# Kernel optimization log

Hardware: AMD Instinct MI355X
Metric: run time of the kernel (lower is better)

The kernel has to match this reference:

```python
import jax, jax.numpy as jnp
import numpy as np

N_HEAD = 16
THETA = 10000.0


def _freqs_cos_sin(head_dim, seq_len):
    # matches precompute_freqs_cis: freqs = 1/theta^(arange(0,dim,2)/dim), outer with t
    inv = 1.0 / (THETA ** (jnp.arange(0, head_dim, 2, dtype=jnp.float32) / head_dim))
    t = jnp.arange(seq_len, dtype=jnp.float32)
    ang = jnp.outer(t, inv)  # [L, head_dim//2]
    return jnp.cos(ang), jnp.sin(ang)


def _rope(x, cos, sin):
    # x: [B, H, L, D]; pairs are interleaved (view_as_complex on (..., D//2, 2))
    x1 = x[..., 0::2]
    x2 = x[..., 1::2]
    out_re = x1 * cos - x2 * sin
    out_im = x1 * sin + x2 * cos
    return jnp.stack([out_re, out_im], axis=-1).reshape(x.shape)


def setup_inputs() -> dict:
    key = jax.random.key(0)
    ks = jax.random.split(key, 11)
    B, L, D = 2, 2048, 1024
    s = 0.02
    return {
        "q": jax.random.normal(ks[0], (B, L, D), jnp.float32),
        "k": jax.random.normal(ks[1], (B, L, D), jnp.float32),
        "v": jax.random.normal(ks[2], (B, L, D), jnp.float32),
        "wq": jax.random.normal(ks[3], (D, D), jnp.float32) * s,
        "bq": jax.random.normal(ks[4], (D,), jnp.float32) * s,
        "wk": jax.random.normal(ks[5], (D, D), jnp.float32) * s,
        "bk": jax.random.normal(ks[6], (D,), jnp.float32) * s,
        "wv": jax.random.normal(ks[7], (D, D), jnp.float32) * s,
        "bv": jax.random.normal(ks[8], (D,), jnp.float32) * s,
        "wo": jax.random.normal(ks[9], (D, D), jnp.float32) * s,
        "bo": jax.random.normal(ks[10], (D,), jnp.float32) * s,
    }


def reference(q, k, v, wq, bq, wk, bk, wv, bv, wo, bo):
    B, L, D = q.shape
    Hd = D // N_HEAD
    # projections (nn.Linear: x @ W^T + b)
    qp = q @ wq.T + bq
    kp = k @ wk.T + bk
    vp = v @ wv.T + bv
    # split: [B, L, D] -> [B, H, L, Hd]
    def split(t):
        return t.reshape(B, L, N_HEAD, Hd).transpose(0, 2, 1, 3)
    qh, kh, vh = split(qp), split(kp), split(vp)
    cos, sin = _freqs_cos_sin(Hd, L)  # [L, Hd//2], broadcasts over B, H
    qh = _rope(qh, cos, sin)
    kh = _rope(kh, cos, sin)
    # scaled dot-product attention (no mask)
    scores = jnp.einsum("bhqd,bhkd->bhqk", qh, kh) / jnp.sqrt(jnp.float32(Hd))
    attn = jax.nn.softmax(scores, axis=-1)
    out = jnp.einsum("bhqk,bhkd->bhqd", attn, vh)
    # concat heads and output projection
    out = out.transpose(0, 2, 1, 3).reshape(B, L, D)
    return out @ wo.T + bo
```

## Files before the change

kernel.cpp:

```cpp
#include <hip/hip_runtime.h>
#include <hip/hip_bf16.h>
#include <math.h>

#define BB 2
#define LL 2048
#define DD 1024
#define NH 16
#define HD 64

typedef short v8s __attribute__((ext_vector_type(8)));
typedef float v4f __attribute__((ext_vector_type(4)));
typedef float v16f __attribute__((ext_vector_type(16)));

__device__ __forceinline__ float b2f(unsigned short b) {
  union { unsigned int u; float f; } c; c.u = ((unsigned int)b) << 16; return c.f;
}
__device__ __forceinline__ unsigned short f2b(float x) {
  union { float f; unsigned int u; } c; c.f = x;
  unsigned int u = c.u;
  u += 0x7fffu + ((u >> 16) & 1u);
  return (unsigned short)(u >> 16);
}
__device__ __forceinline__ unsigned int asu(float x) {
  union { float f; unsigned int u; } c; c.f = x; return c.u;
}
__device__ __forceinline__ unsigned int pk2(float lo, float hi) {
  return __builtin_amdgcn_perm(asu(hi), asu(lo), 0x07060302u);
}

#if defined(__has_builtin)
#if __has_builtin(__builtin_amdgcn_exp2f)
#define EXP2(x) __builtin_amdgcn_exp2f(x)
#else
#define EXP2(x) __expf((x) * 0.69314718056f)
#endif
#else
#define EXP2(x) __expf((x) * 0.69314718056f)
#endif

__device__ __forceinline__ void gload16(const void* g, void* l) {
  __builtin_amdgcn_global_load_lds(
      (const __attribute__((address_space(1))) void*)g,
      (__attribute__((address_space(3))) void*)l, 16, 0, 0);
}

struct CastArgs { const float* s[7]; unsigned short* d[7]; float* ct; float* st; };
__global__ void cast_all(CastArgs a) {
  int z = blockIdx.z;
  if (z == 16) {
    if (blockIdx.x >= 256) return;
    int id = blockIdx.x * blockDim.x + threadIdx.x;
    int t = id >> 5, i = id & 31;
    float inv = powf(10000.0f, -(float)(2 * i) / 64.0f);
    float ang = (float)t * inv;
    a.ct[id] = cosf(ang);
    a.st[id] = sinf(ang);
    return;
  }
  int t = (z < 12) ? (z >> 2) : (z - 9);
  int off = (z < 12) ? ((z & 3) << 18) : 0;
  int i = off + blockIdx.x * blockDim.x + threadIdx.x;
  float4 v = ((const float4*)a.s[t])[i];
  ushort4 o;
  o.x = f2b(v.x); o.y = f2b(v.y); o.z = f2b(v.z); o.w = f2b(v.w);
  ((ushort4*)a.d[t])[i] = o;
}

template <typename OutT>
__device__ __forceinline__ void gemm_body(const unsigned short* __restrict__ X,
                                          const unsigned short* __restrict__ W,
                                          const float* __restrict__ bias,
                                          OutT* __restrict__ Y,
                                          int M, int N, int K) {
  __shared__ __align__(16) unsigned short LDS_[2][16384];
  const int tid = threadIdx.x;
  const int lane = tid & 63, wave = tid >> 6;
  const int quad = lane >> 4, l16 = lane & 15;
  const int bm0 = blockIdx.x * 128;
  const int bn0 = blockIdx.y * 128;
  const int wm = (wave >> 1) * 64, wn = (wave & 1) * 64;

  const v4f vzero = {0.f, 0.f, 0.f, 0.f};
  v4f acc[4][4];
#pragma unroll
  for (int i = 0; i < 4; ++i)
#pragma unroll
    for (int j = 0; j < 4; ++j) acc[i][j] = vzero;

  auto stage = [&](int buf, int k0) {
    unsigned short* As = LDS_[buf];
    unsigned short* Bs = LDS_[buf] + 8192;
#pragma unroll
    for (int c = 0; c < 4; ++c) {
      int id = c * 256 + tid;
      int r = id >> 3, cc = ((id & 7) ^ (r & 7)) * 8;
      gload16(X + (size_t)(bm0 + r) * K + k0 + cc, &As[id * 8]);
    }
#pragma unroll
    for (int c = 0; c < 4; ++c) {
      int id = c * 256 + tid;
      int r = id >> 3, cc = ((id & 7) ^ (r & 7)) * 8;
      gload16(W + (size_t)(bn0 + r) * K + k0 + cc, &Bs[id * 8]);
    }
  };

  stage(0, 0);
  const int nt = K >> 6;
  for (int t = 0; t < nt; ++t) {
    __syncthreads();
    if (t + 1 < nt) stage((t + 1) & 1, (t + 1) << 6);
    const unsigned short* As = LDS_[t & 1];
    const unsigned short* Bs = LDS_[t & 1] + 8192;
#pragma unroll
    for (int kh = 0; kh < 2; ++kh) {
      v8s a[4], b[4];
#pragma unroll
      for (int i = 0; i < 4; ++i) {
        int ra = wm + i * 16 + l16;
        int sa = (kh * 4 + quad) ^ (ra & 7);
        a[i] = *(const v8s*)&As[ra * 64 + sa * 8];
        int rb = wn + i * 16 + l16;
        int sb = (kh * 4 + quad) ^ (rb & 7);
        b[i] = *(const v8s*)&Bs[rb * 64 + sb * 8];
      }
#pragma unroll
      for (int mi = 0; mi < 4; ++mi)
#pragma unroll
        for (int ni = 0; ni < 4; ++ni)
          acc[mi][ni] = __builtin_amdgcn_mfma_f32_16x16x32_bf16(a[mi], b[ni], acc[mi][ni], 0, 0, 0);
    }
  }

  float bv[4];
#pragma unroll
  for (int ni = 0; ni < 4; ++ni) bv[ni] = bias[bn0 + wn + ni * 16 + l16];
#pragma unroll
  for (int mi = 0; mi < 4; ++mi) {
#pragma unroll
    for (int r = 0; r < 4; ++r) {
      int row = bm0 + wm + mi * 16 + quad * 4 + r;
      size_t base = (size_t)row * N + bn0 + wn + l16;
#pragma unroll
      for (int ni = 0; ni < 4; ++ni) {
        float v = acc[mi][ni][r] + bv[ni];
        if constexpr (sizeof(OutT) == 2) {
          Y[base + ni * 16] = (OutT)f2b(v);
        } else {
          Y[base + ni * 16] = (OutT)v;
        }
      }
    }
  }
}

__global__ __launch_bounds__(256) void gemm_qkv(
    const unsigned short* __restrict__ qb, const unsigned short* __restrict__ kb,
    const unsigned short* __restrict__ vb,
    const unsigned short* __restrict__ wqb, const unsigned short* __restrict__ wkb,
    const unsigned short* __restrict__ wvb,
    const float* __restrict__ bq, const float* __restrict__ bk,
    const float* __restrict__ bv_,
    unsigned short* __restrict__ qp, unsigned short* __restrict__ khh,
    unsigned short* __restrict__ vt,
    const float* __restrict__ ctab, const float* __restrict__ stab) {
  __shared__ __align__(16) unsigned short LDS_[2][16384];
  const int z = blockIdx.z;
  const unsigned short* X = (z == 0) ? qb : (z == 1) ? kb : vb;
  const unsigned short* W = (z == 0) ? wqb : (z == 1) ? wkb : wvb;
  const float* bias = (z == 0) ? bq : (z == 1) ? bk : bv_;
  const int K = DD, N = DD;
  const int tid = threadIdx.x;
  const int lane = tid & 63, wave = tid >> 6;
  const int quad = lane >> 4, l16 = lane & 15;
  const int bm0 = blockIdx.x * 128;
  const int bn0 = blockIdx.y * 128;
  const int wm = (wave >> 1) * 64, wn = (wave & 1) * 64;

  const v4f vzero = {0.f, 0.f, 0.f, 0.f};
  v4f acc[4][4];
#pragma unroll
  for (int i = 0; i < 4; ++i)
#pragma unroll
    for (int j = 0; j < 4; ++j) acc[i][j] = vzero;

  auto stage = [&](int buf, int k0) {
    unsigned short* As = LDS_[buf];
    unsigned short* Bs = LDS_[buf] + 8192;
#pragma unroll
    for (int c = 0; c < 4; ++c) {
      int id = c * 256 + tid;
      int r = id >> 3, cc = ((id & 7) ^ (r & 7)) * 8;
      gload16(X + (size_t)(bm0 + r) * K + k0 + cc, &As[id * 8]);
    }
#pragma unroll
    for (int c = 0; c < 4; ++c) {
      int id = c * 256 + tid;
      int r = id >> 3, cc = ((id & 7) ^ (r & 7)) * 8;
      gload16(W + (size_t)(bn0 + r) * K + k0 + cc, &Bs[id * 8]);
    }
  };

  stage(0, 0);
  const int nt = K >> 6;
  for (int t = 0; t < nt; ++t) {
    __syncthreads();
    if (t + 1 < nt) stage((t + 1) & 1, (t + 1) << 6);
    const unsigned short* As = LDS_[t & 1];
    const unsigned short* Bs = LDS_[t & 1] + 8192;
#pragma unroll
    for (int kh = 0; kh < 2; ++kh) {
      v8s a[4], b[4];
#pragma unroll
      for (int i = 0; i < 4; ++i) {
        int ra = wm + i * 16 + l16;
        int sa = (kh * 4 + quad) ^ (ra & 7);
        a[i] = *(const v8s*)&As[ra * 64 + sa * 8];
        int rb = wn + i * 16 + l16;
        int sb = (kh * 4 + quad) ^ (rb & 7);
        b[i] = *(const v8s*)&Bs[rb * 64 + sb * 8];
      }
#pragma unroll
      for (int mi = 0; mi < 4; ++mi)
#pragma unroll
        for (int ni = 0; ni < 4; ++ni)
          acc[mi][ni] = __builtin_amdgcn_mfma_f32_16x16x32_bf16(a[mi], b[ni], acc[mi][ni], 0, 0, 0);
    }
  }

  float bv[4];
#pragma unroll
  for (int ni = 0; ni < 4; ++ni) bv[ni] = bias[bn0 + wn + ni * 16 + l16];

  if (z < 2) {
    const float scl = (z == 0) ? 0.18033688f : 1.0f;
    const int h = (bn0 + wn) >> 6;
    const float sgn = (l16 & 1) ? 1.0f : -1.0f;
#pragma unroll
    for (int mi = 0; mi < 4; ++mi) {
#pragma unroll
      for (int r = 0; r < 4; ++r) {
        int row = bm0 + wm + mi * 16 + quad * 4 + r;
        int l = row & (LL - 1);
        int bidx = row >> 11;
        size_t baseq = (size_t)row * N + bn0 + wn + l16;
        size_t basek = ((size_t)(bidx * NH + h) * LL + l) * HD + l16;
#pragma unroll
        for (int ni = 0; ni < 4; ++ni) {
          int ii = (ni * 16 + l16) >> 1;
          float c = ctab[l * 32 + ii], s = stab[l * 32 + ii];
          float v = acc[mi][ni][r] + bv[ni];
          float vp = __shfl_xor(v, 1);
          float o = (v * c + sgn * (vp * s)) * scl;
          if (z == 0) qp[baseq + ni * 16] = f2b(o);
          else        khh[basek + ni * 16] = f2b(o);
        }
      }
    }
  } else {
    unsigned short* T = LDS_[0];
#pragma unroll
    for (int mi = 0; mi < 4; ++mi)
#pragma unroll
      for (int r = 0; r < 4; ++r) {
        int tl = wm + mi * 16 + quad * 4 + r;
        int tlp = (tl & ~12) | ((tl & 4) << 1) | ((tl & 8) >> 1);
        int chunk = tlp >> 3, offw = tlp & 7;
#pragma unroll
        for (int ni = 0; ni < 4; ++ni) {
          int fl = wn + ni * 16 + l16;
          T[fl * 128 + ((chunk ^ (fl & 15)) * 8) + offw] =
              f2b(acc[mi][ni][r] + bv[ni]);
        }
      }
    __syncthreads();
    int fl = tid >> 1, half = tid & 1;
    int fg = bn0 + fl;
    int h2 = fg >> 6, d = fg & 63;
    int bidx = bm0 >> 11, l0 = bm0 & (LL - 1);
    unsigned short* dst =
        vt + (((size_t)(bidx * NH + h2) * HD + d) * LL) + l0 + half * 64;
#pragma unroll
    for (int i = 0; i < 8; ++i) {
      int chunk = half * 8 + i;
      int slot = chunk ^ (fl & 15);
      *(v8s*)(dst + i * 8) = *(const v8s*)&T[fl * 128 + slot * 8];
    }
  }
}

__global__ __launch_bounds__(256) void gemm_out(
    const unsigned short* x, const unsigned short* w, const float* b, float* y) {
  gemm_body<float>(x, w, b, y, BB * LL, DD, DD);
}

__global__ __launch_bounds__(256, 2) void flash_kernel(
    const unsigned short* __restrict__ qp,
    const unsigned short* __restrict__ kh,
    const unsigned short* __restrict__ vt,
    unsigned short* __restrict__ attn) {
  __shared__ __align__(16) unsigned short S_[2][16384];
  const int tid = threadIdx.x, wave = tid >> 6, lane = tid & 63;
  const int l32 = lane & 31, hf = lane >> 5;
  const int bh = blockIdx.x, b = bh >> 4, hd = bh & 15;
  const int q0 = blockIdx.y * 128;
  const unsigned short* kbase = kh + (size_t)bh * LL * HD;
  const unsigned short* vbase = vt + (size_t)bh * HD * LL;

  const int qrow = q0 + wave * 32 + l32;
  v8s qf[4];
  {
    const unsigned short* qsrc = qp + ((size_t)(b * LL + qrow) * DD + hd * HD);
#pragma unroll
    for (int ks2 = 0; ks2 < 4; ++ks2)
      qf[ks2] = *(const v8s*)(qsrc + ks2 * 16 + hf * 8);
  }

  v16f o0, o1;
#pragma unroll
  for (int i = 0; i < 16; ++i) { o0[i] = 0.0f; o1[i] = 0.0f; }
  float ls = 0.0f;

  {
    unsigned short* Kb = S_[0];
    unsigned short* Vb = S_[0] + 8192;
#pragma unroll
    for (int i = 0; i < 4; ++i) {
      int id = i * 256 + tid;
      int r = id >> 3, c = (id & 7) ^ (r & 7);
      gload16(kbase + (size_t)r * HD + c * 8, &Kb[id * 8]);
    }
#pragma unroll
    for (int i = 0; i < 4; ++i) {
      int id = i * 256 + tid;
      int r = id >> 4, c = (id & 15) ^ (r & 15);
      gload16(vbase + (size_t)r * LL + c * 8, &Vb[id * 8]);
    }
  }

  for (int t = 0; t < 16; ++t) {
    __syncthreads();
    if (t < 15) {
      int kt = (t + 1) * 128;
      unsigned short* Kb = S_[(t + 1) & 1];
      unsigned short* Vb = Kb + 8192;
#pragma unroll
      for (int i = 0; i < 4; ++i) {
        int id = i * 256 + tid;
        int r = id >> 3, c = (id & 7) ^ (r & 7);
        gload16(kbase + (size_t)(kt + r) * HD + c * 8, &Kb[id * 8]);
      }
#pragma unroll
      for (int i = 0; i < 4; ++i) {
        int id = i * 256 + tid;
        int r = id >> 4, c = (id & 15) ^ (r & 15);
        gload16(vbase + (size_t)r * LL + kt + c * 8, &Vb[id * 8]);
      }
    }
    const unsigned short* Ks = S_[t & 1];
    const unsigned short* Vs = Ks + 8192;

#pragma unroll
    for (int g = 0; g < 4; ++g) {
      v16f sc;
#pragma unroll
      for (int i = 0; i < 16; ++i) sc[i] = 0.0f;
#pragma unroll
      for (int ks2 = 0; ks2 < 4; ++ks2) {
        int row = g * 32 + l32;
        int slot = (ks2 * 2 + hf) ^ (lane & 7);
        v8s kf = *(const v8s*)&Ks[row * 64 + slot * 8];
        sc = __builtin_amdgcn_mfma_f32_32x32x16_bf16(kf, qf[ks2], sc, 0, 0, 0);
      }
      v16f e;
#pragma unroll
      for (int i = 0; i < 16; ++i) e[i] = EXP2(sc[i]);
      float t0 = (e[0] + e[1]) + (e[2] + e[3]);
      float t1 = (e[4] + e[5]) + (e[6] + e[7]);
      float t2 = (e[8] + e[9]) + (e[10] + e[11]);
      float t3 = (e[12] + e[13]) + (e[14] + e[15]);
      ls += (t0 + t1) + (t2 + t3);
#pragma unroll
      for (int k2 = 0; k2 < 2; ++k2) {
        union { v8s v; unsigned int u[4]; } pb;
#pragma unroll
        for (int a = 0; a < 4; ++a)
          pb.u[a] = pk2(e[8 * k2 + 2 * a], e[8 * k2 + 2 * a + 1]);
        int k16 = g * 2 + k2;
        int slotv = (k16 * 2 + hf) ^ (lane & 15);
        v8s vf0 = *(const v8s*)&Vs[l32 * 128 + slotv * 8];
        v8s vf1 = *(const v8s*)&Vs[(32 + l32) * 128 + slotv * 8];
        o0 = __builtin_amdgcn_mfma_f32_32x32x16_bf16(vf0, pb.v, o0, 0, 0, 0);
        o1 = __builtin_amdgcn_mfma_f32_32x32x16_bf16(vf1, pb.v, o1, 0, 0, 0);
      }
    }
  }

  ls += __shfl_xor(ls, 32);
  float inv = 1.0f / ls;

  unsigned short* Wt = S_[0] + wave * 2048;
#pragma unroll
  for (int dt = 0; dt < 2; ++dt)
#pragma unroll
    for (int r = 0; r < 16; ++r) {
      int dl = (r & 3) + 8 * (r >> 2) + 4 * hf;
      int d = dt * 32 + dl;
      int chunk = d >> 3, offw = d & 7;
      int slot = chunk ^ (l32 & 7);
      float val = (dt == 0) ? o0[r] : o1[r];
      Wt[l32 * 64 + slot * 8 + offw] = f2b(val * inv);
    }
#pragma unroll
  for (int i = 0; i < 4; ++i) {
    int qr = lane >> 1;
    int chunk = (lane & 1) * 4 + i;
    int slot = chunk ^ (qr & 7);
    v8s dv = *(const v8s*)&Wt[qr * 64 + slot * 8];
    int token = q0 + wave * 32 + qr;
    *(v8s*)(attn + ((size_t)(b * LL + token) * DD) + hd * HD + chunk * 8) = dv;
  }
}

extern "C" void kernel_launch(void* const* d_in, const int* in_sizes, int n_in,
                              void* d_out, int out_size, void* d_ws, size_t ws_size,
                              hipStream_t stream) {
  const float* q  = (const float*)d_in[0];
  const float* k  = (const float*)d_in[1];
  const float* v  = (const float*)d_in[2];
  const float* wq = (const float*)d_in[3];
  const float* bq = (const float*)d_in[4];
  const float* wk = (const float*)d_in[5];
  const float* bk = (const float*)d_in[6];
  const float* wv = (const float*)d_in[7];
  const float* bv = (const float*)d_in[8];
  const float* wo = (const float*)d_in[9];
  const float* bo = (const float*)d_in[10];
  float* out = (float*)d_out;

  size_t off = 0;
  char* wsb = (char*)d_ws;
  auto take = [&](size_t n) { void* p = wsb + off; off += n; return p; };
  const size_t SZT = (size_t)BB * LL * DD * 2;
  const size_t SZW = (size_t)DD * DD * 2;
  unsigned short* qb   = (unsigned short*)take(SZT);
  unsigned short* kb   = (unsigned short*)take(SZT);
  unsigned short* vb   = (unsigned short*)take(SZT);
  unsigned short* wqb  = (unsigned short*)take(SZW);
  unsigned short* wkb  = (unsigned short*)take(SZW);
  unsigned short* wvb  = (unsigned short*)take(SZW);
  unsigned short* wob  = (unsigned short*)take(SZW);
  unsigned short* qp   = (unsigned short*)take(SZT);
  unsigned short* khh  = (unsigned short*)take(SZT);
  unsigned short* vtt  = (unsigned short*)take(SZT);
  unsigned short* attn = (unsigned short*)take(SZT);
  float* ctab = (float*)take((size_t)LL * 32 * 4);
  float* stab = (float*)take((size_t)LL * 32 * 4);

  CastArgs ca;
  ca.s[0] = q;  ca.s[1] = k;  ca.s[2] = v;  ca.s[3] = wq;
  ca.s[4] = wk; ca.s[5] = wv; ca.s[6] = wo;
  ca.d[0] = qb;  ca.d[1] = kb;  ca.d[2] = vb;  ca.d[3] = wqb;
  ca.d[4] = wkb; ca.d[5] = wvb; ca.d[6] = wob;
  ca.ct = ctab; ca.st = stab;
  cast_all<<<dim3(1024, 1, 17), 256, 0, stream>>>(ca);

  gemm_qkv<<<dim3(BB * LL / 128, DD / 128, 3), 256, 0, stream>>>(
      qb, kb, vb, wqb, wkb, wvb, bq, bk, bv, qp, khh, vtt, ctab, stab);

  flash_kernel<<<dim3(BB * NH, LL / 128), 256, 0, stream>>>(
      qp, khh, vtt, attn);

  gemm_out<<<dim3(BB * LL / 128, DD / 128, 1), 256, 0, stream>>>(attn, wob, bo, out);
}
```

Baseline: 216.7 us.

## Use triple-buffered ring pipeline with explicit vmcnt waits in projection GEMMs

Replaces the double-buffered K=64 staging loop in the QKV and output projection GEMMs with a three-slot ring of K=32 tiles, using a new packed swizzle layout. Waits use explicit s_waitcnt vmcnt(4) plus a raw s_barrier instead of __syncthreads, so one tile's loads stay in flight while another computes. LDS drops to 48KB and launch bounds ask for 3 blocks per CU to raise occupancy. The cost is twice as many barrier steps per K, and correctness now rests on hand-counted vmcnt values.

After: 211.6 us. 2.4% less time.

```diff
diff --git a/kernel.cpp b/kernel.cpp
--- a/kernel.cpp
+++ b/kernel.cpp
@@ -43,6 +43,13 @@
       (const __attribute__((address_space(1))) void*)g,
       (__attribute__((address_space(3))) void*)l, 16, 0, 0);
 }
+
+#define VM_WAIT4 do { asm volatile("s_waitcnt vmcnt(4)" ::: "memory"); \
+                      __builtin_amdgcn_sched_barrier(0); } while (0)
+#define VM_WAIT0 do { asm volatile("s_waitcnt vmcnt(0)" ::: "memory"); \
+                      __builtin_amdgcn_sched_barrier(0); } while (0)
+#define SBAR     do { __builtin_amdgcn_s_barrier(); \
+                      __builtin_amdgcn_sched_barrier(0); } while (0)
 
 struct CastArgs { const float* s[7]; unsigned short* d[7]; float* ct; float* st; };
 __global__ void cast_all(CastArgs a) {
@@ -66,94 +73,87 @@
   ((ushort4*)a.d[t])[i] = o;
 }
 
-template <typename OutT>
-__device__ __forceinline__ void gemm_body(const unsigned short* __restrict__ X,
-                                          const unsigned short* __restrict__ W,
-                                          const float* __restrict__ bias,
-                                          OutT* __restrict__ Y,
-                                          int M, int N, int K) {
-  __shared__ __align__(16) unsigned short LDS_[2][16384];
+__device__ __forceinline__ size_t ring_src_off(int id, int row0, int Kd) {
+  int sr = id >> 3, slot = id & 7;
+  int g = slot ^ (sr & 7);
+  int r = (sr << 1) | (g >> 2), c = g & 3;
+  return (size_t)(row0 + r) * Kd + c * 8;
+}
+__device__ __forceinline__ int ring_frag_off(int row, int quad) {
+  int sr = row >> 1;
+  int slot = (((row & 1) << 2) | quad) ^ (sr & 7);
+  return sr * 64 + slot * 8;
+}
+
+__device__ __forceinline__ void ring_gemm_core(
+    const unsigned short* __restrict__ X, const unsigned short* __restrict__ W,
+    unsigned short* LDS_, int bm0, int bn0, v4f acc[4][4]) {
+  const int K = DD;
   const int tid = threadIdx.x;
   const int lane = tid & 63, wave = tid >> 6;
   const int quad = lane >> 4, l16 = lane & 15;
-  const int bm0 = blockIdx.x * 128;
-  const int bn0 = blockIdx.y * 128;
   const int wm = (wave >> 1) * 64, wn = (wave & 1) * 64;
 
-  const v4f vzero = {0.f, 0.f, 0.f, 0.f};
-  v4f acc[4][4];
-#pragma unroll
-  for (int i = 0; i < 4; ++i)
-#pragma unroll
-    for (int j = 0; j < 4; ++j) acc[i][j] = vzero;
-
-  auto stage = [&](int buf, int k0) {
-    unsigned short* As = LDS_[buf];
-    unsigned short* Bs = LDS_[buf] + 8192;
-#pragma unroll
-    for (int c = 0; c < 4; ++c) {
-      int id = c * 256 + tid;
-      int r = id >> 3, cc = ((id & 7) ^ (r & 7)) * 8;
-      gload16(X + (size_t)(bm0 + r) * K + k0 + cc, &As[id * 8]);
-    }
-#pragma unroll
-    for (int c = 0; c < 4; ++c) {
-      int id = c * 256 + tid;
-      int r = id >> 3, cc = ((id & 7) ^ (r & 7)) * 8;
-      gload16(W + (size_t)(bn0 + r) * K + k0 + cc, &Bs[id * 8]);
-    }
+  const unsigned short* aS0 = X + ring_src_off(tid, bm0, K);
+  const unsigned short* aS1 = X + ring_src_off(256 + tid, bm0, K);
+  const unsigned short* bS0 = W + ring_src_off(tid, bn0, K);
+  const unsigned short* bS1 = W + ring_src_off(256 + tid, bn0, K);
+
+  int aoff[4], boff[4];
+#pragma unroll
+  for (int i = 0; i < 4; ++i) {
+    aoff[i] = ring_frag_off(wm + i * 16 + l16, quad);
+    boff[i] = ring_frag_off(wn + i * 16 + l16, quad);
+  }
+
+  auto stage = [&](int q, int kofs) {
+    unsigned short* Ab = &LDS_[q * 4096];
+    unsigned short* Bb = &LDS_[12288 + q * 4096];
+    gload16(aS0 + kofs, &Ab[tid * 8]);
+    gload16(aS1 + kofs, &Ab[(256 + tid) * 8]);
+    gload16(bS0 + kofs, &Bb[tid * 8]);
+    gload16(bS1 + kofs, &Bb[(256 + tid) * 8]);
   };
-
+  auto compute = [&](int q) {
+    const unsigned short* Ab = &LDS_[q * 4096];
+    const unsigned short* Bb = &LDS_[12288 + q * 4096];
+    v8s a[4], b[4];
+#pragma unroll
+    for (int i = 0; i < 4; ++i) {
+      a[i] = *(const v8s*)&Ab[aoff[i]];
+      b[i] = *(const v8s*)&Bb[boff[i]];
+    }
+#pragma unroll
+    for (int mi = 0; mi < 4; ++mi)
+#pragma unroll
+      for (int ni = 0; ni < 4; ++ni)
+        acc[mi][ni] = __builtin_amdgcn_mfma_f32_16x16x32_bf16(a[mi], b[ni], acc[mi][ni], 0, 0, 0);
+  };
+
+  const int nt = K / 32;
   stage(0, 0);
-  const int nt = K >> 6;
-  for (int t = 0; t < nt; ++t) {
-    __syncthreads();
-    if (t + 1 < nt) stage((t + 1) & 1, (t + 1) << 6);
-    const unsigned short* As = LDS_[t & 1];
-    const unsigned short* Bs = LDS_[t & 1] + 8192;
-#pragma unroll
-    for (int kh = 0; kh < 2; ++kh) {
-      v8s a[4], b[4];
-#pragma unroll
-      for (int i = 0; i < 4; ++i) {
-        int ra = wm + i * 16 + l16;
-        int sa = (kh * 4 + quad) ^ (ra & 7);
-        a[i] = *(const v8s*)&As[ra * 64 + sa * 8];
-        int rb = wn + i * 16 + l16;
-        int sb = (kh * 4 + quad) ^ (rb & 7);
-        b[i] = *(const v8s*)&Bs[rb * 64 + sb * 8];
-      }
-#pragma unroll
-      for (int mi = 0; mi < 4; ++mi)
-#pragma unroll
-        for (int ni = 0; ni < 4; ++ni)
-          acc[mi][ni] = __builtin_amdgcn_mfma_f32_16x16x32_bf16(a[mi], b[ni], acc[mi][ni], 0, 0, 0);
-    }
-  }
-
-  float bv[4];
-#pragma unroll
-  for (int ni = 0; ni < 4; ++ni) bv[ni] = bias[bn0 + wn + ni * 16 + l16];
-#pragma unroll
-  for (int mi = 0; mi < 4; ++mi) {
-#pragma unroll
-    for (int r = 0; r < 4; ++r) {
-      int row = bm0 + wm + mi * 16 + quad * 4 + r;
-      size_t base = (size_t)row * N + bn0 + wn + l16;
-#pragma unroll
-      for (int ni = 0; ni < 4; ++ni) {
-        float v = acc[mi][ni][r] + bv[ni];
-        if constexpr (sizeof(OutT) == 2) {
-          Y[base + ni * 16] = (OutT)f2b(v);
-        } else {
-          Y[base + ni * 16] = (OutT)v;
-        }
-      }
-    }
-  }
-}
-
-__global__ __launch_bounds__(256) void gemm_qkv(
+  stage(1, 32);
+  VM_WAIT4;
+  SBAR;
+  int cur = 0, s2 = 2, kofs = 64;
+#pragma unroll 1
+  for (int t = 0; t < nt - 2; ++t) {
+    stage(s2, kofs);
+    compute(cur);
+    VM_WAIT4;
+    SBAR;
+    cur = (cur == 2) ? 0 : cur + 1;
+    s2 = (s2 == 2) ? 0 : s2 + 1;
+    kofs += 32;
+  }
+  compute(cur);
+  VM_WAIT0;
+  SBAR;
+  cur = (cur == 2) ? 0 : cur + 1;
+  compute(cur);
+}
+
+__global__ __launch_bounds__(256, 3) void gemm_qkv(
     const unsigned short* __restrict__ qb, const unsigned short* __restrict__ kb,
     const unsigned short* __restrict__ vb,
     const unsigned short* __restrict__ wqb, const unsigned short* __restrict__ wkb,
@@ -163,12 +163,12 @@
     unsigned short* __restrict__ qp, unsigned short* __restrict__ khh,
     unsigned short* __restrict__ vt,
     const float* __restrict__ ctab, const float* __restrict__ stab) {
-  __shared__ __align__(16) unsigned short LDS_[2][16384];
+  __shared__ __align__(16) unsigned short LDS_[24576];
   const int z = blockIdx.z;
   const unsigned short* X = (z == 0) ? qb : (z == 1) ? kb : vb;
   const unsigned short* W = (z == 0) ? wqb : (z == 1) ? wkb : wvb;
   const float* bias = (z == 0) ? bq : (z == 1) ? bk : bv_;
-  const int K = DD, N = DD;
+  const int N = DD;
   const int tid = threadIdx.x;
   const int lane = tid & 63, wave = tid >> 6;
   const int quad = lane >> 4, l16 = lane & 15;
@@ -183,49 +183,7 @@
 #pragma unroll
     for (int j = 0; j < 4; ++j) acc[i][j] = vzero;
 
-  auto stage = [&](int buf, int k0) {
-    unsigned short* As = LDS_[buf];
-    unsigned short* Bs = LDS_[buf] + 8192;
-#pragma unroll
-    for (int c = 0; c < 4; ++c) {
-      int id = c * 256 + tid;
-      int r = id >> 3, cc = ((id & 7) ^ (r & 7)) * 8;
-      gload16(X + (size_t)(bm0 + r) * K + k0 + cc, &As[id * 8]);
-    }
-#pragma unroll
-    for (int c = 0; c < 4; ++c) {
-      int id = c * 256 + tid;
-      int r = id >> 3, cc = ((id & 7) ^ (r & 7)) * 8;
-      gload16(W + (size_t)(bn0 + r) * K + k0 + cc, &Bs[id * 8]);
-    }
-  };
-
-  stage(0, 0);
-  const int nt = K >> 6;
-  for (int t = 0; t < nt; ++t) {
-    __syncthreads();
-    if (t + 1 < nt) stage((t + 1) & 1, (t + 1) << 6);
-    const unsigned short* As = LDS_[t & 1];
-    const unsigned short* Bs = LDS_[t & 1] + 8192;
-#pragma unroll
-    for (int kh = 0; kh < 2; ++kh) {
-      v8s a[4], b[4];
-#pragma unroll
-      for (int i = 0; i < 4; ++i) {
-        int ra = wm + i * 16 + l16;
-        int sa = (kh * 4 + quad) ^ (ra & 7);
-        a[i] = *(const v8s*)&As[ra * 64 + sa * 8];
-        int rb = wn + i * 16 + l16;
-        int sb = (kh * 4 + quad) ^ (rb & 7);
-        b[i] = *(const v8s*)&Bs[rb * 64 + sb * 8];
-      }
-#pragma unroll
-      for (int mi = 0; mi < 4; ++mi)
-#pragma unroll
-        for (int ni = 0; ni < 4; ++ni)
-          acc[mi][ni] = __builtin_amdgcn_mfma_f32_16x16x32_bf16(a[mi], b[ni], acc[mi][ni], 0, 0, 0);
-    }
-  }
+  ring_gemm_core(X, W, LDS_, bm0, bn0, acc);
 
   float bv[4];
 #pragma unroll
@@ -257,7 +215,8 @@
       }
     }
   } else {
-    unsigned short* T = LDS_[0];
+    __syncthreads();
+    unsigned short* T = LDS_;
 #pragma unroll
     for (int mi = 0; mi < 4; ++mi)
 #pragma unroll
@@ -288,9 +247,41 @@
   }
 }
 
-__global__ __launch_bounds__(256) void gemm_out(
-    const unsigned short* x, const unsigned short* w, const float* b, float* y) {
-  gemm_body<float>(x, w, b, y, BB * LL, DD, DD);
+__global__ __launch_bounds__(256, 3) void gemm_out(
+    const unsigned short* __restrict__ x, const unsigned short* __restrict__ w,
+    const float* __restrict__ b, float* __restrict__ y) {
+  __shared__ __align__(16) unsigned short LDS_[24576];
+  const int N = DD;
+  const int tid = threadIdx.x;
+  const int lane = tid & 63, wave = tid >> 6;
+  const int quad = lane >> 4, l16 = lane & 15;
+  const int bm0 = blockIdx.x * 128;
+  const int bn0 = blockIdx.y * 128;
+  const int wm = (wave >> 1) * 64, wn = (wave & 1) * 64;
+
+  const v4f vzero = {0.f, 0.f, 0.f, 0.f};
+  v4f acc[4][4];
+#pragma unroll
+  for (int i = 0; i < 4; ++i)
+#pragma unroll
+    for (int j = 0; j < 4; ++j) acc[i][j] = vzero;
+
+  ring_gemm_core(x, w, LDS_, bm0, bn0, acc);
+
+  float bv[4];
+#pragma unroll
+  for (int ni = 0; ni < 4; ++ni) bv[ni] = b[bn0 + wn + ni * 16 + l16];
+#pragma unroll
+  for (int mi = 0; mi < 4; ++mi) {
+#pragma unroll
+    for (int r = 0; r < 4; ++r) {
+      int row = bm0 + wm + mi * 16 + quad * 4 + r;
+      size_t base = (size_t)row * N + bn0 + wn + l16;
+#pragma unroll
+      for (int ni = 0; ni < 4; ++ni)
+        y[base + ni * 16] = acc[mi][ni][r] + bv[ni];
+    }
+  }
 }
 
 __global__ __launch_bounds__(256, 2) void flash_kernel(
```
